# Optimization experiments

Measured on AMD Instinct MI355X. Metric: run time of the kernel, lower is better.

The kernel has to match this reference:

```python
import jax, jax.numpy as jnp
import numpy as np

S_RANGE = 15
BLOCK = 4


def _avg_pool(x, k, stride):
    # x: [B,H,W,C], VALID padding (keras AveragePooling2D default)
    s = jax.lax.reduce_window(x, 0.0, jax.lax.add,
                              (1, k, k, 1), (1, stride, stride, 1), 'VALID')
    return s / float(k * k)


def setup_inputs() -> dict:
    key = jax.random.key(0)
    k1, k2 = jax.random.split(key)
    B, H, W, C = 4, 128, 128, 128
    features_0 = jax.random.normal(k1, (B, H, W, C), dtype=jnp.float32)
    features_0from1 = jax.random.normal(k2, (B, H, W, C), dtype=jnp.float32)
    return {"features_0": features_0, "features_0from1": features_0from1}


def reference(features_0, features_0from1):
    B, H, W, C = features_0.shape
    Hc, Wc = H // BLOCK, W // BLOCK

    # f_c: AvgPool(4, stride 4) -> [B,Hc,Wc,C]
    f_c = _avg_pool(features_0, BLOCK, BLOCK)
    # f_r: AvgPool(4, stride 1, VALID) -> [B,H-3,W-3,C]
    f_r = _avg_pool(features_0from1, BLOCK, 1)

    # tf.image.extract_patches(15x15, stride 4, SAME) zero-pads (S_RANGE-1)/2=7 each side
    pad = (S_RANGE - 1) // 2
    f_r_pad = jnp.pad(f_r, ((0, 0), (pad, S_RANGE - 1 - pad),
                            (pad, S_RANGE - 1 - pad), (0, 0)))

    # Gather all 15x15 windows at stride 4: patches[b,i,u,j,v,c] = f_r_pad[b,4i+u,4j+v,c]
    idx_h = BLOCK * jnp.arange(Hc)[:, None] + jnp.arange(S_RANGE)[None, :]  # [Hc,15]
    idx_w = BLOCK * jnp.arange(Wc)[:, None] + jnp.arange(S_RANGE)[None, :]  # [Wc,15]
    patches = f_r_pad[:, idx_h]           # [B,Hc,15,Wpad,C]
    patches = patches[:, :, :, idx_w]     # [B,Hc,15,Wc,15,C]

    # cost: mean over channels of f_c[b,i,j,:] * window values -> [B,15,15,Hc,Wc]
    corr = jnp.einsum('bijc,biujvc->buvij', f_c, patches) / C
    corr = jax.nn.leaky_relu(corr, 0.1)

    # nearest-neighbor upsample by BLOCK; displacement d = u*S_RANGE + v goes last
    cv = jnp.repeat(jnp.repeat(corr, BLOCK, axis=3), BLOCK, axis=4)  # [B,15,15,H,W]
    cv = cv.reshape(B, S_RANGE * S_RANGE, H, W).transpose(0, 2, 3, 1)  # [B,H,W,225]
    return cv
```

## Files before the change

kernel.cpp:

```cpp
#include <hip/hip_runtime.h>
#include <hip/hip_bf16.h>

#define B_   4
#define Hf   128
#define Wf   128
#define HC   32
#define WC   32
#define SR   15
#define PAD  7
#define FR   125
#define FRP  139

typedef float vfloat4 __attribute__((ext_vector_type(4)));

static __device__ __forceinline__ unsigned short f2bf(float x) {
    __hip_bfloat16 h = __float2bfloat16(x);
    unsigned short u; __builtin_memcpy(&u, &h, 2); return u;
}

static __device__ __forceinline__ float mrg(float x, float y, bool hi, int m) {
    float u0 = hi ? x : y;
    float t  = __shfl_xor(u0, m, 64);
    return (hi ? y : x) + t;
}

__global__ __launch_bounds__(256) void pool_fused(const float* __restrict__ in0,
                                                  const float* __restrict__ in1,
                                                  float* __restrict__ fc,
                                                  unsigned short* __restrict__ fr16) {
    int bid = blockIdx.x;
    if (bid < 4 * 18 * 18) {
        int yt = bid % 18;
        int xt = (bid / 18) % 18;
        int b  = bid / (18 * 18);
        int c4 = threadIdx.x & 31;
        int x  = xt * 8 + (threadIdx.x >> 5);
        if (x >= FRP) return;
        int y0 = yt * 8;
        bool xin = (x >= PAD) && (x < PAD + FR);

        float4 h[11];
        if (xin) {
            int xi = x - PAD;
            const float4* base = reinterpret_cast<const float4*>(in1) + (b * Hf * Wf) * 32 + c4;
#pragma unroll
            for (int k = 0; k < 11; ++k) {
                int r = y0 - PAD + k;
                r = r < 0 ? 0 : (r > Hf - 1 ? Hf - 1 : r);
                float4 s = make_float4(0.f, 0.f, 0.f, 0.f);
#pragma unroll
                for (int dx = 0; dx < 4; ++dx) {
                    float4 v = base[(r * Wf + xi + dx) * 32];
                    s.x += v.x; s.y += v.y; s.z += v.z; s.w += v.w;
                }
                h[k] = s;
            }
        }
        const float s = 1.0f / 16.0f;
        ushort4* fr4 = reinterpret_cast<ushort4*>(fr16);
#pragma unroll
        for (int yy = 0; yy < 8; ++yy) {
            int y = y0 + yy;
            if (y >= FRP) continue;
            ushort4 o = make_ushort4(0, 0, 0, 0);
            if (xin && y >= PAD && y < PAD + FR) {
                o.x = f2bf((h[yy].x + h[yy+1].x + h[yy+2].x + h[yy+3].x) * s);
                o.y = f2bf((h[yy].y + h[yy+1].y + h[yy+2].y + h[yy+3].y) * s);
                o.z = f2bf((h[yy].z + h[yy+1].z + h[yy+2].z + h[yy+3].z) * s);
                o.w = f2bf((h[yy].w + h[yy+1].w + h[yy+2].w + h[yy+3].w) * s);
            }
            fr4[((b * FRP + y) * FRP + x) * 32 + c4] = o;
        }
    } else {
        int t = (bid - 4 * 18 * 18) * 256 + threadIdx.x;
        int c4 = t & 31;
        int j  = (t >> 5) & 31;
        int i  = (t >> 10) & 31;
        int b  = t >> 15;
        const float4* in = reinterpret_cast<const float4*>(in0);
        int base = ((b * Hf + 4 * i) * Wf + 4 * j) * 32 + c4;
        float4 acc = make_float4(0.f, 0.f, 0.f, 0.f);
#pragma unroll
        for (int dy = 0; dy < 4; ++dy)
#pragma unroll
            for (int dx = 0; dx < 4; ++dx) {
                float4 v = in[base + dy * (Wf * 32) + dx * 32];
                acc.x += v.x; acc.y += v.y; acc.z += v.z; acc.w += v.w;
            }
        const float sc = 1.0f / 16.0f;
        acc.x *= sc; acc.y *= sc; acc.z *= sc; acc.w *= sc;
        reinterpret_cast<float4*>(fc)[t] = acc;
    }
}

__global__ __launch_bounds__(256) void corr_kernel(const float* __restrict__ fc,
                                                   const unsigned short* __restrict__ fr16,
                                                   float* __restrict__ out) {
    int blk  = blockIdx.x;
    int cell = (blk & 7) * 512 + (blk >> 3);
    int j = cell & 31;
    int i = (cell >> 5) & 31;
    int b = cell >> 10;

    int tid = threadIdx.x;
    int g   = tid >> 5;
    int gl  = tid & 31;

    __shared__ float corr_rep[900];

    float4 f = reinterpret_cast<const float4*>(fc)[((b * HC + i) * WC + j) * 32 + gl];

    const uint2* frbase = reinterpret_cast<const uint2*>(fr16);
    bool h16 = gl & 16, h8 = gl & 8, h4 = gl & 4, h2 = gl & 2;
    int vidx = ((gl >> 4) & 1) * 8 + ((gl >> 3) & 1) * 4 + ((gl >> 2) & 1) * 2 + ((gl >> 1) & 1);

#pragma unroll
    for (int pass = 0; pass < 2; ++pass) {
        int u = g + pass * 8;
        if (u < SR) {
            int row = 4 * i + u;
            const uint2* p = frbase + ((b * FRP + row) * FRP + 4 * j) * 32 + gl;

            float a[16];
#pragma unroll
            for (int k = 0; k < 16; ++k) a[k] = 0.f;
#pragma unroll
            for (int v = 0; v < SR; ++v) {
                uint2 w = p[v * 32];
                float r0 = __uint_as_float(w.x << 16);
                float r1 = __uint_as_float(w.x & 0xffff0000u);
                float r2 = __uint_as_float(w.y << 16);
                float r3 = __uint_as_float(w.y & 0xffff0000u);
                a[v] = fmaf(f.x, r0, fmaf(f.y, r1, fmaf(f.z, r2, f.w * r3)));
            }

            float bb[8], cc[4], dd[2], e;
#pragma unroll
            for (int k = 0; k < 8; ++k) bb[k] = mrg(a[k], a[k + 8], h16, 16);
#pragma unroll
            for (int k = 0; k < 4; ++k) cc[k] = mrg(bb[k], bb[k + 4], h8, 8);
#pragma unroll
            for (int k = 0; k < 2; ++k) dd[k] = mrg(cc[k], cc[k + 2], h4, 4);
            e = mrg(dd[0], dd[1], h2, 2);
            e += __shfl_xor(e, 1, 64);

            if (vidx < SR) {
                float cv = e * (1.0f / 128.0f);
                float val = cv > 0.f ? cv : 0.1f * cv;
                int uvq = u * SR + vidx;
                int c0 = (gl & 1) * 225;
                corr_rep[c0 + uvq] = val;
                corr_rep[c0 + 450 + uvq] = val;
            }
        }
    }
    __syncthreads();

    if (tid < SR * SR) {
        vfloat4 val = *reinterpret_cast<const vfloat4*>(&corr_rep[4 * tid]);
        vfloat4* out4 = reinterpret_cast<vfloat4*>(out);
        long pix   = (long)(b * Hf + 4 * i) * Wf + 4 * j;
        long base4 = pix * (SR * SR) / 4;
#pragma unroll
        for (int di = 0; di < 4; ++di)
            __builtin_nontemporal_store(val, &out4[base4 + di * (Wf * SR * SR / 4) + tid]);
    }
}

extern "C" void kernel_launch(void* const* d_in, const int* in_sizes, int n_in,
                              void* d_out, int out_size, void* d_ws, size_t ws_size,
                              hipStream_t stream) {
    const float* f0 = (const float*)d_in[0];
    const float* f1 = (const float*)d_in[1];
    float* out = (float*)d_out;

    float* fc = (float*)d_ws;
    unsigned short* fr16 = (unsigned short*)(fc + B_ * HC * WC * 128);

    pool_fused<<<4 * 18 * 18 + 512, 256, 0, stream>>>(f0, f1, fc, fr16);
    corr_kernel<<<B_ * HC * WC, 256, 0, stream>>>(fc, fr16, out);
}
```

Measured before the change: 45.34 us.

## Compute correlation with bf16 MFMA over 8-cell strips using LDS-staged rows

```diff
diff --git a/kernel.cpp b/kernel.cpp
--- a/kernel.cpp
+++ b/kernel.cpp
@@ -8,26 +8,21 @@
 #define WC   32
 #define SR   15
 #define PAD  7
-#define FR   125
-#define FRP  139
+#define FRR  139
+#define FRW  144
 
-typedef float vfloat4 __attribute__((ext_vector_type(4)));
+typedef float  vfloat4 __attribute__((ext_vector_type(4)));
+typedef short  short8  __attribute__((ext_vector_type(8)));
 
 static __device__ __forceinline__ unsigned short f2bf(float x) {
     __hip_bfloat16 h = __float2bfloat16(x);
     unsigned short u; __builtin_memcpy(&u, &h, 2); return u;
 }
 
-static __device__ __forceinline__ float mrg(float x, float y, bool hi, int m) {
-    float u0 = hi ? x : y;
-    float t  = __shfl_xor(u0, m, 64);
-    return (hi ? y : x) + t;
-}
-
 __global__ __launch_bounds__(256) void pool_fused(const float* __restrict__ in0,
                                                   const float* __restrict__ in1,
-                                                  float* __restrict__ fc,
-                                                  unsigned short* __restrict__ fr16) {
+                                                  unsigned short* __restrict__ fc,
+                                                  unsigned short* __restrict__ fr) {
     int bid = blockIdx.x;
     if (bid < 4 * 18 * 18) {
         int yt = bid % 18;
@@ -35,14 +30,13 @@
         int b  = bid / (18 * 18);
         int c4 = threadIdx.x & 31;
         int x  = xt * 8 + (threadIdx.x >> 5);
-        if (x >= FRP) return;
         int y0 = yt * 8;
-        bool xin = (x >= PAD) && (x < PAD + FR);
+        bool xin = (x >= PAD) && (x < PAD + 125);
 
         float4 h[11];
         if (xin) {
             int xi = x - PAD;
-            const float4* base = reinterpret_cast<const float4*>(in1) + (b * Hf * Wf) * 32 + c4;
+            const float4* base = reinterpret_cast<const float4*>(in1) + (size_t)(b * Hf * Wf) * 32 + c4;
 #pragma unroll
             for (int k = 0; k < 11; ++k) {
                 int r = y0 - PAD + k;
@@ -50,26 +44,26 @@
                 float4 s = make_float4(0.f, 0.f, 0.f, 0.f);
 #pragma unroll
                 for (int dx = 0; dx < 4; ++dx) {
-                    float4 v = base[(r * Wf + xi + dx) * 32];
+                    float4 v = base[(size_t)(r * Wf + xi + dx) * 32];
                     s.x += v.x; s.y += v.y; s.z += v.z; s.w += v.w;
                 }
                 h[k] = s;
             }
         }
-        const float s = 1.0f / 16.0f;
-        ushort4* fr4 = reinterpret_cast<ushort4*>(fr16);
+        const float sc = 1.0f / 16.0f;
+        ushort4* fr4 = reinterpret_cast<ushort4*>(fr);
 #pragma unroll
         for (int yy = 0; yy < 8; ++yy) {
             int y = y0 + yy;
-            if (y >= FRP) continue;
+            if (y >= FRR) continue;
             ushort4 o = make_ushort4(0, 0, 0, 0);
-            if (xin && y >= PAD && y < PAD + FR) {
-                o.x = f2bf((h[yy].x + h[yy+1].x + h[yy+2].x + h[yy+3].x) * s);
-                o.y = f2bf((h[yy].y + h[yy+1].y + h[yy+2].y + h[yy+3].y) * s);
-                o.z = f2bf((h[yy].z + h[yy+1].z + h[yy+2].z + h[yy+3].z) * s);
-                o.w = f2bf((h[yy].w + h[yy+1].w + h[yy+2].w + h[yy+3].w) * s);
+            if (xin && y >= PAD && y < PAD + 125) {
+                o.x = f2bf((h[yy].x + h[yy+1].x + h[yy+2].x + h[yy+3].x) * sc);
+                o.y = f2bf((h[yy].y + h[yy+1].y + h[yy+2].y + h[yy+3].y) * sc);
+                o.z = f2bf((h[yy].z + h[yy+1].z + h[yy+2].z + h[yy+3].z) * sc);
+                o.w = f2bf((h[yy].w + h[yy+1].w + h[yy+2].w + h[yy+3].w) * sc);
             }
-            fr4[((b * FRP + y) * FRP + x) * 32 + c4] = o;
+            fr4[((size_t)(b * FRR + y) * FRW + x) * 32 + c4] = o;
         }
     } else {
         int t = (bid - 4 * 18 * 18) * 256 + threadIdx.x;
@@ -78,7 +72,7 @@
         int i  = (t >> 10) & 31;
         int b  = t >> 15;
         const float4* in = reinterpret_cast<const float4*>(in0);
-        int base = ((b * Hf + 4 * i) * Wf + 4 * j) * 32 + c4;
+        size_t base = ((size_t)(b * Hf + 4 * i) * Wf + 4 * j) * 32 + c4;
         float4 acc = make_float4(0.f, 0.f, 0.f, 0.f);
 #pragma unroll
         for (int dy = 0; dy < 4; ++dy)
@@ -88,82 +82,99 @@
                 acc.x += v.x; acc.y += v.y; acc.z += v.z; acc.w += v.w;
             }
         const float sc = 1.0f / 16.0f;
-        acc.x *= sc; acc.y *= sc; acc.z *= sc; acc.w *= sc;
-        reinterpret_cast<float4*>(fc)[t] = acc;
+        ushort4 o;
+        o.x = f2bf(acc.x * sc); o.y = f2bf(acc.y * sc);
+        o.z = f2bf(acc.z * sc); o.w = f2bf(acc.w * sc);
+        reinterpret_cast<ushort4*>(fc)[t] = o;
     }
 }
 
-__global__ __launch_bounds__(256) void corr_kernel(const float* __restrict__ fc,
-                                                   const unsigned short* __restrict__ fr16,
-                                                   float* __restrict__ out) {
+__global__ __launch_bounds__(192) void corr_mfma(const unsigned short* __restrict__ fc,
+                                                 const unsigned short* __restrict__ fr,
+                                                 float* __restrict__ out) {
     int blk  = blockIdx.x;
-    int cell = (blk & 7) * 512 + (blk >> 3);
-    int j = cell & 31;
-    int i = (cell >> 5) & 31;
-    int b = cell >> 10;
+    int cell = (blk & 7) * 64 + (blk >> 3);
+    int jq = cell & 3;
+    int i  = (cell >> 2) & 31;
+    int b  = cell >> 7;
+    int j0 = jq * 8;
 
-    int tid = threadIdx.x;
-    int g   = tid >> 5;
-    int gl  = tid & 31;
+    int tid  = threadIdx.x;
+    int lane = tid & 63;
+    int wv   = tid >> 6;
 
-    __shared__ float corr_rep[900];
+    __shared__ __align__(16) unsigned short stage[3][6144];
+    __shared__ __align__(16) float rep[8][900];
 
-    float4 f = reinterpret_cast<const float4*>(fc)[((b * HC + i) * WC + j) * 32 + gl];
+    const short8* fc8 = reinterpret_cast<const short8*>(fc);
+    int arow = (b * HC + i) * WC + j0 + (lane & 15);
+    short8 afrag[4];
+#pragma unroll
+    for (int kk = 0; kk < 4; ++kk)
+        afrag[kk] = fc8[(size_t)arow * 16 + kk * 4 + (lane >> 4)];
+    asm volatile("s_waitcnt vmcnt(0)" ::: "memory");
 
-    const uint2* frbase = reinterpret_cast<const uint2*>(fr16);
-    bool h16 = gl & 16, h8 = gl & 8, h4 = gl & 4, h2 = gl & 2;
-    int vidx = ((gl >> 4) & 1) * 8 + ((gl >> 3) & 1) * 4 + ((gl >> 2) & 1) * 2 + ((gl >> 1) & 1);
+    auto STAGE = [&](int u, int bi) {
+        const char* gsrc = (const char*)(fr + ((size_t)((b * FRR + 4 * i + u) * FRW) + 4 * j0) * 128);
+        char* lbase = (char*)&stage[bi][0];
+#pragma unroll
+        for (int k = 0; k < 4; ++k) {
+            int d   = k * 3072 + tid * 16;
+            int src = d ^ (((d >> 8) & 7) << 4);
+            __builtin_amdgcn_global_load_lds(
+                (const __attribute__((address_space(1))) unsigned int*)(gsrc + src),
+                (__attribute__((address_space(3))) unsigned int*)(lbase + d), 16, 0, 0);
+        }
+    };
+
+    STAGE(0, 0);
+    STAGE(1, 1);
+    const float lrs = 1.0f / 128.0f;
 
 #pragma unroll
-    for (int pass = 0; pass < 2; ++pass) {
-        int u = g + pass * 8;
-        if (u < SR) {
-            int row = 4 * i + u;
-            const uint2* p = frbase + ((b * FRP + row) * FRP + 4 * j) * 32 + gl;
+    for (int u = 0; u < 15; ++u) {
+        __builtin_amdgcn_s_barrier();
+        __builtin_amdgcn_sched_barrier(0);
+        if (u < 13) {
+            STAGE(u + 2, (u + 2) % 3);
+            asm volatile("s_waitcnt vmcnt(8)" ::: "memory");
+        } else if (u == 13) {
+            asm volatile("s_waitcnt vmcnt(4)" ::: "memory");
+        } else {
+            asm volatile("s_waitcnt vmcnt(0)" ::: "memory");
+        }
 
-            float a[16];
+        const char* sb = (const char*)&stage[u % 3][0];
+        vfloat4 acc = {0.f, 0.f, 0.f, 0.f};
 #pragma unroll
-            for (int k = 0; k < 16; ++k) a[k] = 0.f;
+        for (int kk = 0; kk < 4; ++kk) {
+            int lin  = wv * 4096 + (lane & 15) * 256 + (lane >> 4) * 16 + kk * 64;
+            int addr = lin ^ ((lane & 7) << 4);
+            short8 bfrag = *reinterpret_cast<const short8*>(sb + addr);
+            acc = __builtin_amdgcn_mfma_f32_16x16x32_bf16(afrag[kk], bfrag, acc, 0, 0, 0);
+        }
 #pragma unroll
-            for (int v = 0; v < SR; ++v) {
-                uint2 w = p[v * 32];
-                float r0 = __uint_as_float(w.x << 16);
-                float r1 = __uint_as_float(w.x & 0xffff0000u);
-                float r2 = __uint_as_float(w.y << 16);
-                float r3 = __uint_as_float(w.y & 0xffff0000u);
-                a[v] = fmaf(f.x, r0, fmaf(f.y, r1, fmaf(f.z, r2, f.w * r3)));
-            }
-
-            float bb[8], cc[4], dd[2], e;
-#pragma unroll
-            for (int k = 0; k < 8; ++k) bb[k] = mrg(a[k], a[k + 8], h16, 16);
-#pragma unroll
-            for (int k = 0; k < 4; ++k) cc[k] = mrg(bb[k], bb[k + 4], h8, 8);
-#pragma unroll
-            for (int k = 0; k < 2; ++k) dd[k] = mrg(cc[k], cc[k + 2], h4, 4);
-            e = mrg(dd[0], dd[1], h2, 2);
-            e += __shfl_xor(e, 1, 64);
-
-            if (vidx < SR) {
-                float cv = e * (1.0f / 128.0f);
-                float val = cv > 0.f ? cv : 0.1f * cv;
-                int uvq = u * SR + vidx;
-                int c0 = (gl & 1) * 225;
-                corr_rep[c0 + uvq] = val;
-                corr_rep[c0 + 450 + uvq] = val;
+        for (int r = 0; r < 4; ++r) {
+            int jrow = (lane >> 4) * 4 + r;
+            int v    = wv * 16 + (lane & 15) - 4 * jrow;
+            if (jrow < 8 && v >= 0 && v < SR) {
+                float c   = acc[r] * lrs;
+                float val = c > 0.f ? c : 0.1f * c;
+                float* rp = &rep[jrow][u * SR + v];
+                rp[0] = val; rp[225] = val; rp[450] = val; rp[675] = val;
             }
         }
     }
     __syncthreads();
 
-    if (tid < SR * SR) {
-        vfloat4 val = *reinterpret_cast<const vfloat4*>(&corr_rep[4 * tid]);
-        vfloat4* out4 = reinterpret_cast<vfloat4*>(out);
-        long pix   = (long)(b * Hf + 4 * i) * Wf + 4 * j;
-        long base4 = pix * (SR * SR) / 4;
+    const vfloat4* rep4 = reinterpret_cast<const vfloat4*>(&rep[0][0]);
+    vfloat4* out4 = reinterpret_cast<vfloat4*>(out);
+    size_t orow0 = ((size_t)(b * Hf + 4 * i) * Wf + 4 * j0) * 225 / 4;
+    for (int q = tid; q < 1800; q += 192) {
+        vfloat4 val = rep4[q];
 #pragma unroll
         for (int di = 0; di < 4; ++di)
-            __builtin_nontemporal_store(val, &out4[base4 + di * (Wf * SR * SR / 4) + tid]);
+            __builtin_nontemporal_store(val, &out4[orow0 + (size_t)di * (Wf * 225 / 4) + q]);
     }
 }
 
@@ -174,9 +185,9 @@
     const float* f1 = (const float*)d_in[1];
     float* out = (float*)d_out;
 
-    float* fc = (float*)d_ws;
-    unsigned short* fr16 = (unsigned short*)(fc + B_ * HC * WC * 128);
+    unsigned short* fc = (unsigned short*)d_ws;
+    unsigned short* fr = fc + (size_t)B_ * HC * WC * 128;
 
-    pool_fused<<<4 * 18 * 18 + 512, 256, 0, stream>>>(f0, f1, fc, fr16);
-    corr_kernel<<<B_ * HC * WC, 256, 0, stream>>>(fc, fr16, out);
+    pool_fused<<<4 * 18 * 18 + 512, 256, 0, stream>>>(f0, f1, fc, fr);
+    corr_mfma<<<B_ * 32 * 4, 192, 0, stream>>>(fc, fr, out);
 }
```

Result: no change. 45.53 us (+0.4%).
